# Optimization experiments

Measured on AMD Instinct MI355X. Metric: run time of the kernel, lower is better.

Reference implementation:

```python
import jax, jax.numpy as jnp
import numpy as np

GRID_SIZE = 5
SPLINE_ORDER = 3
NUM_EXPERTS = 8
TOP_K = 2
CAP_FACTOR = 1.25
TEMP = 1.0
GDHW = (4, 4, 4)


def make_grid(in_features):
    # efficient-KAN grid buffer: grid_range=[-1,1], extended by spline_order on each side
    h = 2.0 / GRID_SIZE
    g = jnp.arange(-SPLINE_ORDER, GRID_SIZE + SPLINE_ORDER + 1, dtype=jnp.float32) * h - 1.0
    return jnp.broadcast_to(g, (in_features, g.shape[0]))


def b_splines(x, grid):
    # x: (N, in) -> (N, in, GRID_SIZE + SPLINE_ORDER) Cox-de Boor bases
    x = x[:, :, None]
    bases = ((x >= grid[:, :-1]) & (x < grid[:, 1:])).astype(x.dtype)
    for k in range(1, SPLINE_ORDER + 1):
        left = (x - grid[:, : -(k + 1)]) / (grid[:, k:-1] - grid[:, : -(k + 1)])
        right = (grid[:, k + 1:] - x) / (grid[:, k + 1:] - grid[:, 1:-k])
        bases = left * bases[:, :, :-1] + right * bases[:, :, 1:]
    return bases


def kan_linear(x, base_w, spline_w, scaler, grid):
    base = jax.nn.silu(x) @ base_w.T
    bs = b_splines(x, grid)                                   # (N, in, coef)
    spline = jnp.einsum('nic,oic->no', bs, spline_w * scaler[:, :, None])
    return base + spline


def layernorm(x, w, b, eps=1e-5):
    mu = x.mean(-1, keepdims=True)
    var = x.var(-1, keepdims=True)
    return (x - mu) / jnp.sqrt(var + eps) * w + b


def setup_inputs() -> dict:
    key = jax.random.key(0)
    ks = jax.random.split(key, 12)
    Cf, hidden, E, nc = 256, 170, NUM_EXPERTS, 2
    coef = GRID_SIZE + SPLINE_ORDER
    def nrm(k, shape, scale):
        return jax.random.normal(k, shape, dtype=jnp.float32) * scale
    return {
        'fpn_feat': nrm(ks[0], (8, 254, 32, 32, 32), 1.0),
        'seg_logits': nrm(ks[1], (8, 2, 32, 32, 32), 1.0),
        'ln_r_w': jnp.ones((Cf,), jnp.float32),
        'ln_r_b': jnp.zeros((Cf,), jnp.float32),
        'ln_h_w': jnp.ones((Cf,), jnp.float32),
        'ln_h_b': jnp.zeros((Cf,), jnp.float32),
        'router_w': nrm(ks[2], (E, Cf), Cf ** -0.5),
        'router_b': jnp.zeros((E,), jnp.float32),
        'bw1': nrm(ks[3], (E, hidden, Cf), Cf ** -0.5),
        'sw1': nrm(ks[4], (E, hidden, Cf, coef), 0.1 * Cf ** -0.5),
        'sc1': nrm(ks[5], (E, hidden, Cf), Cf ** -0.5),
        'bw2': nrm(ks[6], (E, Cf, hidden), hidden ** -0.5),
        'sw2': nrm(ks[7], (E, Cf, hidden, coef), 0.1 * hidden ** -0.5),
        'sc2': nrm(ks[8], (E, Cf, hidden), hidden ** -0.5),
        'cls_bw': nrm(ks[9], (nc, Cf), Cf ** -0.5),
        'cls_sw': nrm(ks[10], (nc, Cf, coef), 0.1 * Cf ** -0.5),
        'cls_sc': nrm(ks[11], (nc, Cf), Cf ** -0.5),
        'grid_cf': make_grid(Cf),
        'grid_hid': make_grid(hidden),
    }


def reference(fpn_feat, seg_logits, ln_r_w, ln_r_b, ln_h_w, ln_h_b,
              router_w, router_b, bw1, sw1, sc1, bw2, sw2, sc2,
              cls_bw, cls_sw, cls_sc, grid_cf, grid_hid):
    fused = jnp.concatenate([fpn_feat, seg_logits], axis=1)   # (B, Cf, D, H, W)
    B, C, D, H, W = fused.shape
    gd, gh, gw = GDHW
    dp, hp, wp = D // gd, H // gh, W // gw
    # split into gd*gh*gw blocks per sample
    blk = fused.reshape(B, C, gd, dp, gh, hp, gw, wp)
    blk = blk.transpose(0, 2, 4, 6, 1, 3, 5, 7).reshape(-1, C, dp, hp, wp)
    vec = blk.mean(axis=(2, 3, 4))                            # (N, Cf) global avg pool

    N = vec.shape[0]
    E = NUM_EXPERTS
    x_norm = layernorm(vec, ln_r_w, ln_r_b)
    scores = (x_norm @ router_w.T + router_b) / TEMP          # (N, E)
    top_val, top_idx = jax.lax.top_k(scores, TOP_K)
    top_w = jax.nn.softmax(top_val, axis=-1)
    capacity = int(CAP_FACTOR * N * TOP_K / E) + 1

    onehot = top_idx[None] == jnp.arange(E)[:, None, None]    # (E, N, K)
    sel = onehot.any(-1)                                      # (E, N)
    pos = jnp.cumsum(sel.astype(jnp.int32), axis=1)           # rank among selected (1-based)
    keep = sel & (pos <= capacity)                            # capacity drop = first-come order
    w = (top_w[None] * onehot.astype(top_w.dtype)).sum(-1)    # (E, N) combine weights

    def expert(bw1e, sw1e, sc1e, bw2e, sw2e, sc2e):
        h = kan_linear(x_norm, bw1e, sw1e, sc1e, grid_cf)
        h = jax.nn.gelu(h, approximate=False)                 # torch nn.GELU default (erf)
        return kan_linear(h, bw2e, sw2e, sc2e, grid_hid)

    y_all = jax.vmap(expert)(bw1, sw1, sc1, bw2, sw2, sc2)    # (E, N, Cf)
    out = jnp.einsum('en,enc->nc', keep.astype(vec.dtype) * w, y_all)

    conf = scores.max(-1)                                     # (N,)
    logits_blk = kan_linear(layernorm(out, ln_h_w, ln_h_b), cls_bw, cls_sw, cls_sc, grid_cf)
    P = gd * gh * gw
    weight = jax.nn.softmax(conf.reshape(B, P), axis=-1)[:, :, None]
    logits = (logits_blk.reshape(B, P, -1) * weight).sum(1)   # (B, num_classes)
    return logits
```

## Files before the change

kernel.cpp:

```cpp
#include <hip/hip_runtime.h>
#include <math.h>

#define CF 256
#define HID 170
#define NE 8
#define NTOK 512
#define K1 2304
#define K2P 1536
#define CAPACITY 161

typedef __bf16 bf16x8 __attribute__((ext_vector_type(8)));
typedef unsigned short u16x8 __attribute__((ext_vector_type(8)));
typedef float f32x4 __attribute__((ext_vector_type(4)));

__device__ __forceinline__ float silu_f(float x) { return x / (1.0f + expf(-x)); }
__device__ __forceinline__ float gelu_f(float x) {
    return 0.5f * x * (1.0f + erff(x * 0.70710678118654752f));
}

__device__ __forceinline__ unsigned short f2bf(float f) {
    unsigned int u = __float_as_uint(f);
    u = u + 0x7fffu + ((u >> 16) & 1u);
    return (unsigned short)(u >> 16);
}

__device__ __forceinline__ void bspline8(float x, float bs[8]) {
    float b[11];
#pragma unroll
    for (int j = 0; j < 11; ++j) {
        float g0 = (float)(j - 3) * 0.4f - 1.0f;
        float g1 = (float)(j - 2) * 0.4f - 1.0f;
        b[j] = (x >= g0 && x < g1) ? 1.0f : 0.0f;
    }
#pragma unroll
    for (int k = 1; k <= 3; ++k) {
        float inv = 2.5f / (float)k;
#pragma unroll
        for (int j = 0; j < 10 - (k - 1); ++j) {
            float gj   = (float)(j - 3) * 0.4f - 1.0f;
            float gjk1 = (float)(j - 2 + k) * 0.4f - 1.0f;
            b[j] = (x - gj) * inv * b[j] + (gjk1 - x) * inv * b[j + 1];
        }
    }
#pragma unroll
    for (int c = 0; c < 8; ++c) bs[c] = b[c];
}

__global__ __launch_bounds__(256) void mega_front_kernel(const float* __restrict__ fpn,
                                                         const float* __restrict__ seg,
                                                         const float* __restrict__ bw1,
                                                         const float* __restrict__ sw1,
                                                         const float* __restrict__ sc1,
                                                         const float* __restrict__ bw2,
                                                         const float* __restrict__ sw2,
                                                         const float* __restrict__ sc2,
                                                         float* __restrict__ vec,
                                                         unsigned short* __restrict__ W1,
                                                         unsigned short* __restrict__ W2,
                                                         float* __restrict__ out) {
    int id = blockIdx.x, tid = threadIdx.x;
    if (id == 2048 && tid < 16) out[tid] = 0.0f;
    if (id < 2048) {
        int c = id & 255, b = id >> 8;
        const float* src = (c < 254) ? fpn + (size_t)(b * 254 + c) * 32768
                                     : seg + (size_t)(b * 2 + (c - 254)) * 32768;
        const float4* s4 = (const float4*)src;
        float s[4] = {0.f, 0.f, 0.f, 0.f};
#pragma unroll
        for (int it = 0; it < 32; ++it) {
            float4 v = s4[it * 256 + tid];
            s[it >> 3] += v.x + v.y + v.z + v.w;
        }
        __shared__ float acc[64];
        if (tid < 64) acc[tid] = 0.0f;
        __syncthreads();
        int bh = tid >> 6, bw = (tid & 7) >> 1;
#pragma unroll
        for (int bd = 0; bd < 4; ++bd) atomicAdd(&acc[bd * 16 + bh * 4 + bw], s[bd]);
        __syncthreads();
        if (tid < 64) vec[(size_t)(b * 64 + tid) * CF + c] = acc[tid] * (1.0f / 512.0f);
    } else if (id < 2048 + NE * HID) {
        int r = id - 2048;
        int o = r % HID, e = r / HID, i = tid;
        size_t oi = (size_t)(e * HID + o) * CF + i;
        unsigned short* row = W1 + (size_t)(e * HID + o) * K1;
        row[i] = f2bf(bw1[oi]);
        float sc = sc1[oi];
        const float* sw = sw1 + oi * 8;
        u16x8 pk;
#pragma unroll
        for (int c = 0; c < 8; ++c) pk[c] = f2bf(sw[c] * sc);
        *(u16x8*)(row + CF + i * 8) = pk;
    } else {
        int r = id - (2048 + NE * HID);
        int o = r & 255, e = r >> 8, t = tid;
        unsigned short* row = W2 + (size_t)(e * CF + o) * K2P;
        if (t < HID) {
            size_t oi = (size_t)(e * CF + o) * HID + t;
            row[t] = f2bf(bw2[oi]);
            float sc = sc2[oi];
            const float* sw = sw2 + oi * 8;
            u16x8 pk;
#pragma unroll
            for (int c = 0; c < 8; ++c) pk[c] = f2bf(sw[c] * sc);
            *(u16x8*)(row + HID + t * 8) = pk;
        } else if (t < HID + 6) {
            row[HID * 9 + (t - HID)] = 0;
        }
    }
}

__global__ __launch_bounds__(256) void ln_score_a1_kernel(const float* __restrict__ vec,
                                                          const float* __restrict__ lnw,
                                                          const float* __restrict__ lnb,
                                                          const float* __restrict__ rw,
                                                          const float* __restrict__ rb,
                                                          float* __restrict__ scores,
                                                          unsigned short* __restrict__ A1,
                                                          unsigned short* __restrict__ A2) {
    int n = blockIdx.x, i = threadIdx.x;
    if (i < 48) {
        int e = i / 6, j = i - e * 6;
        A2[((size_t)e * NTOK + n) * K2P + HID * 9 + j] = 0;
    }
    float v = vec[(size_t)n * CF + i];
    float s1 = v, s2 = v * v;
#pragma unroll
    for (int off = 32; off > 0; off >>= 1) {
        s1 += __shfl_xor(s1, off);
        s2 += __shfl_xor(s2, off);
    }
    __shared__ float rs1[4], rs2[4];
    int lane = i & 63, wid = i >> 6;
    if (lane == 0) { rs1[wid] = s1; rs2[wid] = s2; }
    __syncthreads();
    float tot1 = rs1[0] + rs1[1] + rs1[2] + rs1[3];
    float tot2 = rs2[0] + rs2[1] + rs2[2] + rs2[3];
    float mu = tot1 * (1.0f / CF);
    float var = tot2 * (1.0f / CF) - mu * mu;
    float rsd = rsqrtf(var + 1e-5f);
    float xv = (v - mu) * rsd * lnw[i] + lnb[i];
    unsigned short* r = A1 + (size_t)n * K1;
    r[i] = f2bf(silu_f(xv));
    float bs[8]; bspline8(xv, bs);
    u16x8 pk;
#pragma unroll
    for (int c = 0; c < 8; ++c) pk[c] = f2bf(bs[c]);
    *(u16x8*)(r + CF + i * 8) = pk;
    float p[NE];
#pragma unroll
    for (int e = 0; e < NE; ++e) p[e] = xv * rw[e * CF + i];
#pragma unroll
    for (int off = 32; off > 0; off >>= 1)
#pragma unroll
        for (int e = 0; e < NE; ++e) p[e] += __shfl_xor(p[e], off);
    __shared__ float pacc[4][NE];
    if (lane == 0)
#pragma unroll
        for (int e = 0; e < NE; ++e) pacc[wid][e] = p[e];
    __syncthreads();
    if (i < NE)
        scores[n * NE + i] = pacc[0][i] + pacc[1][i] + pacc[2][i] + pacc[3][i] + rb[i];
}

template <int MODE>
__global__ __launch_bounds__(128) void gemm_mfma_kernel(
        const unsigned short* __restrict__ Ag, const unsigned short* __restrict__ Bg,
        float* __restrict__ C, unsigned short* __restrict__ A2,
        const float* __restrict__ scores, float* __restrict__ cw, float* __restrict__ conf,
        int N, int K, long sA, long sB, long sC, int ldc, int ntx, int grid_main) {
    __shared__ alignas(16) unsigned char smem[12288];
    int bid = blockIdx.x, tid = threadIdx.x;
    int lane = tid & 63, w = tid >> 6;

    if (MODE == 1 && bid >= grid_main) {
        int* ti0 = (int*)smem;
        int* ti1 = ti0 + NTOK;
        float* tw0 = (float*)(ti1 + NTOK);
        float* tw1 = tw0 + NTOK;
#pragma unroll
        for (int q = 0; q < 4; ++q) {
            int t = q * 128 + tid;
            float m1 = -1e30f, m2 = -1e30f; int i1 = 0, i2 = 0;
#pragma unroll
            for (int e = 0; e < NE; ++e) {
                float sc = scores[t * NE + e];
                if (sc > m1) { m2 = m1; i2 = i1; m1 = sc; i1 = e; }
                else if (sc > m2) { m2 = sc; i2 = e; }
            }
            conf[t] = m1;
            float ew = expf(m2 - m1);
            ti0[t] = i1; ti1[t] = i2;
            tw0[t] = 1.0f / (1.0f + ew); tw1[t] = ew / (1.0f + ew);
        }
        __syncthreads();
#pragma unroll
        for (int eh = 0; eh < 4; ++eh) {
            int e = w * 4 + eh;
            int cnt = 0;
#pragma unroll
            for (int c = 0; c < NTOK / 64; ++c) {
                int t = c * 64 + lane;
                int h0 = (ti0[t] == e), h1 = (ti1[t] == e);
                int sel = h0 | h1;
                unsigned long long mask = __ballot(sel);
                int pos = cnt + (int)__popcll(mask & ((1ull << lane) - 1ull));
                float wv = 0.f;
                if (sel && pos < CAPACITY) wv = h0 ? tw0[t] : tw1[t];
                cw[e * NTOK + t] = wv;
                cnt += (int)__popcll(mask);
            }
        }
        return;
    }

    int tpe = 16 * ntx;
    int e = bid / tpe, rem = bid % tpe;
    int m0 = (rem / ntx) * 32, n0 = (rem % ntx) * 64;
    const unsigned short* A = Ag + (size_t)e * sA + (size_t)m0 * K;
    const unsigned short* B = Bg + (size_t)e * sB + (size_t)n0 * K;

    unsigned char* AsB = smem;
    unsigned char* BsB = smem + 4096;

    int fr = lane & 15, fg = lane >> 4;
    int aw[2], bw[4];
    const unsigned short* aSrc[2];
    const unsigned short* bSrc[4];
    bool bOk[4];
#pragma unroll
    for (int q = 0; q < 2; ++q) {
        int c = tid + q * 128, r = c >> 3, ch = c & 7;
        aw[q] = r * 128 + ((ch * 16) ^ ((r & 7) << 4));
        aSrc[q] = A + (size_t)r * K + ch * 8;
    }
#pragma unroll
    for (int q = 0; q < 4; ++q) {
        int c = tid + q * 128, r = c >> 3, ch = c & 7;
        bw[q] = r * 128 + ((ch * 16) ^ ((r & 7) << 4));
        bSrc[q] = B + (size_t)r * K + ch * 8;
        bOk[q] = (n0 + r) < N;
    }

    f32x4 acc[2][2];
#pragma unroll
    for (int i = 0; i < 2; ++i)
#pragma unroll
        for (int j = 0; j < 2; ++j)
#pragma unroll
            for (int r = 0; r < 4; ++r) acc[i][j][r] = 0.f;

    const int steps = K >> 6;
    u16x8 pa[2], pb[4];
#pragma unroll
    for (int q = 0; q < 2; ++q) pa[q] = *(const u16x8*)aSrc[q];
#pragma unroll
    for (int q = 0; q < 4; ++q)
        pb[q] = bOk[q] ? *(const u16x8*)bSrc[q] : (u16x8){0, 0, 0, 0, 0, 0, 0, 0};

    for (int s = 0; s < steps; ++s) {
        __syncthreads();
#pragma unroll
        for (int q = 0; q < 2; ++q) *(u16x8*)(AsB + aw[q]) = pa[q];
#pragma unroll
        for (int q = 0; q < 4; ++q) *(u16x8*)(BsB + bw[q]) = pb[q];
        __syncthreads();
        if (s + 1 < steps) {
            int k0 = (s + 1) << 6;
#pragma unroll
            for (int q = 0; q < 2; ++q) pa[q] = *(const u16x8*)(aSrc[q] + k0);
#pragma unroll
            for (int q = 0; q < 4; ++q)
                if (bOk[q]) pb[q] = *(const u16x8*)(bSrc[q] + k0);
        }
#pragma unroll
        for (int ks = 0; ks < 2; ++ks) {
            int kb = ks * 64 + fg * 16;
            u16x8 af[2], bf[2];
#pragma unroll
            for (int mf = 0; mf < 2; ++mf) {
                int row = mf * 16 + fr;
                af[mf] = *(const u16x8*)(AsB + row * 128 + (kb ^ ((row & 7) << 4)));
            }
#pragma unroll
            for (int nf = 0; nf < 2; ++nf) {
                int row = w * 32 + nf * 16 + fr;
                bf[nf] = *(const u16x8*)(BsB + row * 128 + (kb ^ ((row & 7) << 4)));
            }
#pragma unroll
            for (int mf = 0; mf < 2; ++mf)
#pragma unroll
                for (int nf = 0; nf < 2; ++nf)
                    acc[mf][nf] = __builtin_amdgcn_mfma_f32_16x16x32_bf16(
                        __builtin_bit_cast(bf16x8, af[mf]),
                        __builtin_bit_cast(bf16x8, bf[nf]), acc[mf][nf], 0, 0, 0);
        }
    }

    if (MODE == 1) {
#pragma unroll
        for (int mf = 0; mf < 2; ++mf)
#pragma unroll
            for (int nf = 0; nf < 2; ++nf)
#pragma unroll
                for (int r = 0; r < 4; ++r) {
                    int row = m0 + mf * 16 + fg * 4 + r;
                    int col = n0 + w * 32 + nf * 16 + fr;
                    if (col < N) {
                        float g = gelu_f(acc[mf][nf][r]);
                        unsigned short* rr = A2 + ((size_t)e * NTOK + row) * K2P;
                        rr[col] = f2bf(silu_f(g));
                        float bs[8]; bspline8(g, bs);
                        u16x8 pk;
#pragma unroll
                        for (int c = 0; c < 8; ++c) pk[c] = f2bf(bs[c]);
                        *(u16x8*)(rr + HID + col * 8) = pk;
                    }
                }
    } else {
        float* Ce = C + (size_t)e * sC;
#pragma unroll
        for (int mf = 0; mf < 2; ++mf)
#pragma unroll
            for (int nf = 0; nf < 2; ++nf)
#pragma unroll
                for (int r = 0; r < 4; ++r) {
                    int row = m0 + mf * 16 + fg * 4 + r;
                    int col = n0 + w * 32 + nf * 16 + fr;
                    if (col < N) Ce[(size_t)row * ldc + col] = acc[mf][nf][r];
                }
    }
}

__global__ __launch_bounds__(256) void combcls_kernel(const float* __restrict__ y,
                                                      const float* __restrict__ cw,
                                                      const float* __restrict__ conf,
                                                      const float* __restrict__ lnw,
                                                      const float* __restrict__ lnb,
                                                      const float* __restrict__ cbw,
                                                      const float* __restrict__ csw,
                                                      const float* __restrict__ csc,
                                                      float* __restrict__ out) {
    int n = blockIdx.x, i = threadIdx.x;
    float v = 0.f;
#pragma unroll
    for (int e = 0; e < NE; ++e)
        v += cw[e * NTOK + n] * y[((size_t)(e * NTOK + n)) * CF + i];
    float s1 = v, s2 = v * v;
#pragma unroll
    for (int off = 32; off > 0; off >>= 1) {
        s1 += __shfl_xor(s1, off);
        s2 += __shfl_xor(s2, off);
    }
    __shared__ float rA[4], rB[4], rP0[4], rP1[4];
    int lane = i & 63, wid = i >> 6;
    if (lane == 0) { rA[wid] = s1; rB[wid] = s2; }
    __syncthreads();
    float tot1 = rA[0] + rA[1] + rA[2] + rA[3];
    float tot2 = rB[0] + rB[1] + rB[2] + rB[3];
    float mu = tot1 * (1.0f / CF);
    float var = tot2 * (1.0f / CF) - mu * mu;
    float rs = rsqrtf(var + 1e-5f);
    float xh = (v - mu) * rs * lnw[i] + lnb[i];
    float si = silu_f(xh);
    float bs[8]; bspline8(xh, bs);
    float p0 = si * cbw[i], p1 = si * cbw[CF + i];
    float sp0 = 0.f, sp1 = 0.f;
#pragma unroll
    for (int c = 0; c < 8; ++c) {
        sp0 += bs[c] * csw[(size_t)i * 8 + c];
        sp1 += bs[c] * csw[(size_t)(CF + i) * 8 + c];
    }
    p0 += sp0 * csc[i];
    p1 += sp1 * csc[CF + i];
#pragma unroll
    for (int off = 32; off > 0; off >>= 1) {
        p0 += __shfl_xor(p0, off);
        p1 += __shfl_xor(p1, off);
    }
    if (lane == 0) { rP0[wid] = p0; rP1[wid] = p1; }
    __syncthreads();
    if (i < 64) {
        int b = n >> 6;
        float cf = conf[b * 64 + i];
        float mx = cf;
#pragma unroll
        for (int off = 32; off > 0; off >>= 1) mx = fmaxf(mx, __shfl_xor(mx, off));
        float ev = expf(cf - mx);
        float sum = ev;
#pragma unroll
        for (int off = 32; off > 0; off >>= 1) sum += __shfl_xor(sum, off);
        if (i == 0) {
            float wself = expf(conf[n] - mx) / sum;
            float l0 = rP0[0] + rP0[1] + rP0[2] + rP0[3];
            float l1 = rP1[0] + rP1[1] + rP1[2] + rP1[3];
            atomicAdd(&out[b * 2 + 0], wself * l0);
            atomicAdd(&out[b * 2 + 1], wself * l1);
        }
    }
}

extern "C" void kernel_launch(void* const* d_in, const int* in_sizes, int n_in,
                              void* d_out, int out_size, void* d_ws, size_t ws_size,
                              hipStream_t stream) {
    const float* fpn      = (const float*)d_in[0];
    const float* seg      = (const float*)d_in[1];
    const float* ln_r_w   = (const float*)d_in[2];
    const float* ln_r_b   = (const float*)d_in[3];
    const float* ln_h_w   = (const float*)d_in[4];
    const float* ln_h_b   = (const float*)d_in[5];
    const float* router_w = (const float*)d_in[6];
    const float* router_b = (const float*)d_in[7];
    const float* bw1      = (const float*)d_in[8];
    const float* sw1      = (const float*)d_in[9];
    const float* sc1      = (const float*)d_in[10];
    const float* bw2      = (const float*)d_in[11];
    const float* sw2      = (const float*)d_in[12];
    const float* sc2      = (const float*)d_in[13];
    const float* cls_bw   = (const float*)d_in[14];
    const float* cls_sw   = (const float*)d_in[15];
    const float* cls_sc   = (const float*)d_in[16];
    float* out = (float*)d_out;

    float* ws = (float*)d_ws;
    float* vec    = ws;
    float* scores = vec + 131072;
    float* cw     = scores + 4096;
    float* conf   = cw + 4096;
    float* yall   = conf + 512;
    unsigned short* A1b = (unsigned short*)(yall + 1048576);
    unsigned short* W1b = A1b + (size_t)NTOK * K1;
    unsigned short* A2b = W1b + (size_t)NE * HID * K1;
    unsigned short* W2b = A2b + (size_t)NE * NTOK * K2P;

    mega_front_kernel<<<dim3(2048 + NE * HID + 2048), dim3(256), 0, stream>>>(
        fpn, seg, bw1, sw1, sc1, bw2, sw2, sc2, vec, W1b, W2b, out);
    ln_score_a1_kernel<<<dim3(NTOK), dim3(256), 0, stream>>>(vec, ln_r_w, ln_r_b, router_w,
                                                             router_b, scores, A1b, A2b);
    gemm_mfma_kernel<1><<<dim3(385), dim3(128), 0, stream>>>(
        A1b, W1b, nullptr, A2b, scores, cw, conf, HID, K1, 0L, (long)HID * K1, 0L, 0,
        3, 384);
    gemm_mfma_kernel<0><<<dim3(512), dim3(128), 0, stream>>>(
        A2b, W2b, yall, nullptr, nullptr, nullptr, nullptr, CF, K2P, (long)NTOK * K2P,
        (long)CF * K2P, (long)NTOK * CF, CF, 4, 512);
    combcls_kernel<<<dim3(NTOK), dim3(256), 0, stream>>>(yall, cw, conf, ln_h_w, ln_h_b,
                                                         cls_bw, cls_sw, cls_sc, out);
}
```

Before: 131.0 us.

## Retile expert GEMMs to 64x64 tiles with 256-wide K steps and 3D grid

Both expert GEMM kernels move from 32x64 tiles with 128 threads and 64-deep K steps to 64x64 tiles with 256 threads (a 2x2 wave layout) and 256-deep K steps, staged through a 64KB LDS buffer. The launch becomes a 3D grid (n-tile, m-tile, expert), and the routing block is folded into the x==3 column of the first GEMM. The goal is more operand reuse per tile and fewer barriers per unit of K. In exchange, the larger LDS footprint and register prefetch buffers lower occupancy, and there are fewer blocks in flight (256 per GEMM).

After: 116.1 us. 11.4% less time.

```diff
diff --git a/kernel.cpp b/kernel.cpp
--- a/kernel.cpp
+++ b/kernel.cpp
@@ -164,23 +164,24 @@
 }
 
 template <int MODE>
-__global__ __launch_bounds__(128) void gemm_mfma_kernel(
+__global__ __launch_bounds__(256) void gemm_mfma_kernel(
         const unsigned short* __restrict__ Ag, const unsigned short* __restrict__ Bg,
         float* __restrict__ C, unsigned short* __restrict__ A2,
         const float* __restrict__ scores, float* __restrict__ cw, float* __restrict__ conf,
-        int N, int K, long sA, long sB, long sC, int ldc, int ntx, int grid_main) {
-    __shared__ alignas(16) unsigned char smem[12288];
-    int bid = blockIdx.x, tid = threadIdx.x;
+        int N, int K, long sA, long sB, long sC, int ldc) {
+    __shared__ alignas(16) unsigned char smem[65536];
+    int tid = threadIdx.x;
     int lane = tid & 63, w = tid >> 6;
 
-    if (MODE == 1 && bid >= grid_main) {
+    if (MODE == 1 && blockIdx.x == 3) {
+        if (blockIdx.y != 0 || blockIdx.z != 0) return;
         int* ti0 = (int*)smem;
         int* ti1 = ti0 + NTOK;
         float* tw0 = (float*)(ti1 + NTOK);
         float* tw1 = tw0 + NTOK;
 #pragma unroll
-        for (int q = 0; q < 4; ++q) {
-            int t = q * 128 + tid;
+        for (int half = 0; half < 2; ++half) {
+            int t = half * 256 + tid;
             float m1 = -1e30f, m2 = -1e30f; int i1 = 0, i2 = 0;
 #pragma unroll
             for (int e = 0; e < NE; ++e) {
@@ -195,8 +196,8 @@
         }
         __syncthreads();
 #pragma unroll
-        for (int eh = 0; eh < 4; ++eh) {
-            int e = w * 4 + eh;
+        for (int e2 = 0; e2 < 2; ++e2) {
+            int e = w * 2 + e2;
             int cnt = 0;
 #pragma unroll
             for (int c = 0; c < NTOK / 64; ++c) {
@@ -214,33 +215,24 @@
         return;
     }
 
-    int tpe = 16 * ntx;
-    int e = bid / tpe, rem = bid % tpe;
-    int m0 = (rem / ntx) * 32, n0 = (rem % ntx) * 64;
-    const unsigned short* A = Ag + (size_t)e * sA + (size_t)m0 * K;
-    const unsigned short* B = Bg + (size_t)e * sB + (size_t)n0 * K;
-
     unsigned char* AsB = smem;
-    unsigned char* BsB = smem + 4096;
-
+    unsigned char* BsB = smem + 32768;
+
+    int e = blockIdx.z;
+    const unsigned short* A = Ag + (size_t)e * sA;
+    const unsigned short* B = Bg + (size_t)e * sB;
+    int m0 = blockIdx.y * 64, n0 = blockIdx.x * 64;
+    int wr = w >> 1, wc = w & 1;
     int fr = lane & 15, fg = lane >> 4;
-    int aw[2], bw[4];
-    const unsigned short* aSrc[2];
-    const unsigned short* bSrc[4];
-    bool bOk[4];
-#pragma unroll
-    for (int q = 0; q < 2; ++q) {
-        int c = tid + q * 128, r = c >> 3, ch = c & 7;
-        aw[q] = r * 128 + ((ch * 16) ^ ((r & 7) << 4));
-        aSrc[q] = A + (size_t)r * K + ch * 8;
-    }
-#pragma unroll
-    for (int q = 0; q < 4; ++q) {
-        int c = tid + q * 128, r = c >> 3, ch = c & 7;
-        bw[q] = r * 128 + ((ch * 16) ^ ((r & 7) << 4));
-        bSrc[q] = B + (size_t)r * K + ch * 8;
-        bOk[q] = (n0 + r) < N;
-    }
+
+    int r0 = tid >> 5, ch = tid & 31;
+    int d0 = r0 * 512 + ((ch * 16) ^ ((r0 & 7) << 4));
+    const unsigned short* aP = A + (size_t)(m0 + r0) * K + ch * 8;
+    const unsigned short* bP = B + (size_t)(n0 + r0) * K + ch * 8;
+    bool bOk[8];
+#pragma unroll
+    for (int q = 0; q < 8; ++q) bOk[q] = (n0 + r0 + q * 8) < N;
+    const u16x8 zero8 = {0, 0, 0, 0, 0, 0, 0, 0};
 
     f32x4 acc[2][2];
 #pragma unroll
@@ -250,42 +242,43 @@
 #pragma unroll
             for (int r = 0; r < 4; ++r) acc[i][j][r] = 0.f;
 
-    const int steps = K >> 6;
-    u16x8 pa[2], pb[4];
-#pragma unroll
-    for (int q = 0; q < 2; ++q) pa[q] = *(const u16x8*)aSrc[q];
-#pragma unroll
-    for (int q = 0; q < 4; ++q)
-        pb[q] = bOk[q] ? *(const u16x8*)bSrc[q] : (u16x8){0, 0, 0, 0, 0, 0, 0, 0};
+    const int steps = K >> 8;
+    u16x8 ra[8], rb[8];
+#pragma unroll
+    for (int q = 0; q < 8; ++q) {
+        ra[q] = *(const u16x8*)(aP + (size_t)q * 8 * K);
+        rb[q] = bOk[q] ? *(const u16x8*)(bP + (size_t)q * 8 * K) : zero8;
+    }
 
     for (int s = 0; s < steps; ++s) {
         __syncthreads();
 #pragma unroll
-        for (int q = 0; q < 2; ++q) *(u16x8*)(AsB + aw[q]) = pa[q];
-#pragma unroll
-        for (int q = 0; q < 4; ++q) *(u16x8*)(BsB + bw[q]) = pb[q];
+        for (int q = 0; q < 8; ++q) {
+            *(u16x8*)(AsB + d0 + q * 4096) = ra[q];
+            *(u16x8*)(BsB + d0 + q * 4096) = rb[q];
+        }
         __syncthreads();
         if (s + 1 < steps) {
-            int k0 = (s + 1) << 6;
-#pragma unroll
-            for (int q = 0; q < 2; ++q) pa[q] = *(const u16x8*)(aSrc[q] + k0);
-#pragma unroll
-            for (int q = 0; q < 4; ++q)
-                if (bOk[q]) pb[q] = *(const u16x8*)(bSrc[q] + k0);
-        }
-#pragma unroll
-        for (int ks = 0; ks < 2; ++ks) {
+            int k0 = (s + 1) << 8;
+#pragma unroll
+            for (int q = 0; q < 8; ++q) {
+                ra[q] = *(const u16x8*)(aP + (size_t)q * 8 * K + k0);
+                rb[q] = bOk[q] ? *(const u16x8*)(bP + (size_t)q * 8 * K + k0) : zero8;
+            }
+        }
+#pragma unroll
+        for (int ks = 0; ks < 8; ++ks) {
             int kb = ks * 64 + fg * 16;
             u16x8 af[2], bf[2];
 #pragma unroll
             for (int mf = 0; mf < 2; ++mf) {
-                int row = mf * 16 + fr;
-                af[mf] = *(const u16x8*)(AsB + row * 128 + (kb ^ ((row & 7) << 4)));
+                int row = wr * 32 + mf * 16 + fr;
+                af[mf] = *(const u16x8*)(AsB + row * 512 + (kb ^ ((row & 7) << 4)));
             }
 #pragma unroll
             for (int nf = 0; nf < 2; ++nf) {
-                int row = w * 32 + nf * 16 + fr;
-                bf[nf] = *(const u16x8*)(BsB + row * 128 + (kb ^ ((row & 7) << 4)));
+                int row = wc * 32 + nf * 16 + fr;
+                bf[nf] = *(const u16x8*)(BsB + row * 512 + (kb ^ ((row & 7) << 4)));
             }
 #pragma unroll
             for (int mf = 0; mf < 2; ++mf)
@@ -304,8 +297,8 @@
             for (int nf = 0; nf < 2; ++nf)
 #pragma unroll
                 for (int r = 0; r < 4; ++r) {
-                    int row = m0 + mf * 16 + fg * 4 + r;
-                    int col = n0 + w * 32 + nf * 16 + fr;
+                    int row = m0 + wr * 32 + mf * 16 + fg * 4 + r;
+                    int col = n0 + wc * 32 + nf * 16 + fr;
                     if (col < N) {
                         float g = gelu_f(acc[mf][nf][r]);
                         unsigned short* rr = A2 + ((size_t)e * NTOK + row) * K2P;
@@ -325,8 +318,8 @@
             for (int nf = 0; nf < 2; ++nf)
 #pragma unroll
                 for (int r = 0; r < 4; ++r) {
-                    int row = m0 + mf * 16 + fg * 4 + r;
-                    int col = n0 + w * 32 + nf * 16 + fr;
+                    int row = m0 + wr * 32 + mf * 16 + fg * 4 + r;
+                    int col = n0 + wc * 32 + nf * 16 + fr;
                     if (col < N) Ce[(size_t)row * ldc + col] = acc[mf][nf][r];
                 }
     }
@@ -437,12 +430,11 @@
         fpn, seg, bw1, sw1, sc1, bw2, sw2, sc2, vec, W1b, W2b, out);
     ln_score_a1_kernel<<<dim3(NTOK), dim3(256), 0, stream>>>(vec, ln_r_w, ln_r_b, router_w,
                                                              router_b, scores, A1b, A2b);
-    gemm_mfma_kernel<1><<<dim3(385), dim3(128), 0, stream>>>(
-        A1b, W1b, nullptr, A2b, scores, cw, conf, HID, K1, 0L, (long)HID * K1, 0L, 0,
-        3, 384);
-    gemm_mfma_kernel<0><<<dim3(512), dim3(128), 0, stream>>>(
+    gemm_mfma_kernel<1><<<dim3(4, 8, NE), dim3(256), 0, stream>>>(
+        A1b, W1b, nullptr, A2b, scores, cw, conf, HID, K1, 0L, (long)HID * K1, 0L, 0);
+    gemm_mfma_kernel<0><<<dim3(4, 8, NE), dim3(256), 0, stream>>>(
         A2b, W2b, yall, nullptr, nullptr, nullptr, nullptr, CF, K2P, (long)NTOK * K2P,
-        (long)CF * K2P, (long)NTOK * CF, CF, 4, 512);
+        (long)CF * K2P, (long)NTOK * CF, CF);
     combcls_kernel<<<dim3(NTOK), dim3(256), 0, stream>>>(yall, cw, conf, ln_h_w, ln_h_b,
                                                          cls_bw, cls_sw, cls_sc, out);
 }
```
